# Optimization experiments

Measured on AMD Instinct MI355X. Metric: run time of the kernel, lower is better.

The kernel has to match this reference:

```python
import jax, jax.numpy as jnp
import numpy as np


def _base_index(H, W, dtype=jnp.float32):
    # Homogeneous pixel coordinates (x, y, 1) per pixel, shape [H, W, 3].
    x = jnp.arange(W, dtype=dtype)
    y = jnp.arange(H, dtype=dtype)
    xx, yy = jnp.meshgrid(x, y)  # [H, W]
    return jnp.stack([xx, yy, jnp.ones_like(xx)], axis=-1)


def _bilinear_resample(image, coords):
    # image: [B, H, W, C]; coords: [B, H, W, 2] in (x, y) order (tf resampler convention).
    # Out-of-bounds corners contribute zero (zero padding), matching tfa.image.resampler.
    B, H, W, C = image.shape
    x = coords[..., 0]
    y = coords[..., 1]
    x0 = jnp.floor(x)
    y0 = jnp.floor(y)
    wx1 = x - x0
    wy1 = y - y0
    wx0 = 1.0 - wx1
    wy0 = 1.0 - wy1
    x0i = x0.astype(jnp.int32)
    y0i = y0.astype(jnp.int32)
    x1i = x0i + 1
    y1i = y0i + 1

    def corner(yi, xi, w):
        valid = (xi >= 0) & (xi < W) & (yi >= 0) & (yi < H)
        xc = jnp.clip(xi, 0, W - 1)
        yc = jnp.clip(yi, 0, H - 1)
        # gather per batch: [B, H, W, C]
        g = jax.vmap(lambda im, yy, xx: im[yy, xx])(image, yc, xc)
        return g * (w * valid.astype(image.dtype))[..., None]

    return (corner(y0i, x0i, wy0 * wx0) + corner(y0i, x1i, wy0 * wx1)
            + corner(y1i, x0i, wy1 * wx0) + corner(y1i, x1i, wy1 * wx1))


def setup_inputs() -> dict:
    key = jax.random.key(0)
    k1, k2, k3 = jax.random.split(key, 3)
    B, H, W, C = 4, 512, 640, 16
    image_tensor = jax.random.normal(k1, (B, H, W, C), dtype=jnp.float32)
    # positive depths around 1
    depth_tensor = 0.5 + jax.random.uniform(k2, (B, H, W), dtype=jnp.float32)
    # near-identity projective transform so sampled coords land mostly in-bounds
    eye = jnp.eye(4, dtype=jnp.float32)[None].repeat(B, axis=0)
    project_tensor = eye + 0.001 * jax.random.normal(k3, (B, 4, 4), dtype=jnp.float32)
    return {"image_tensor": image_tensor, "depth_tensor": depth_tensor,
            "project_tensor": project_tensor}


def reference(image_tensor, depth_tensor, project_tensor):
    B, H, W, C = image_tensor.shape
    base = _base_index(H, W, image_tensor.dtype)  # [H, W, 3]
    R = project_tensor[:, :3, :3]                 # [B, 3, 3]
    t = project_tensor[:, :3, 3]                  # [B, 3]
    # tf.tensordot(R, base, [-1,-1]) -> [B,3,H,W]; transpose -> [B,H,W,3]
    rotate = jnp.einsum('bij,hwj->bhwi', R, base)
    sample = rotate * depth_tensor[..., None] + t[:, None, None, :]  # [B,H,W,3]
    coords = sample[..., :2] / sample[..., 2:3]                       # [B,H,W,2] (x,y)
    return _bilinear_resample(image_tensor, coords)
```

## Files before the change

kernel.cpp:

```cpp
#include <hip/hip_runtime.h>

constexpr int B  = 4;
constexpr int H  = 512;
constexpr int Wd = 640;
constexpr int C  = 16;
constexpr int NPIX = B * H * Wd;
constexpr int NTHREADS = NPIX * (C / 4);

__global__ __launch_bounds__(256) void depth_project_kernel(
    const float* __restrict__ image,
    const float* __restrict__ depth,
    const float* __restrict__ proj,
    float4* __restrict__ out)
{
    int tid = blockIdx.x * blockDim.x + threadIdx.x;
    if (tid >= NTHREADS) return;

    int c4  = tid & 3;
    int pix = tid >> 2;
    int w   = pix % Wd;
    int t   = pix / Wd;
    int h   = t % H;
    int b   = t / H;

    const float* P = proj + b * 16;
    float x = (float)w;
    float y = (float)h;
    float d = depth[pix];

    float sx = (P[0] * x + P[1] * y + P[2])  * d + P[3];
    float sy = (P[4] * x + P[5] * y + P[6])  * d + P[7];
    float sz = (P[8] * x + P[9] * y + P[10]) * d + P[11];
    float cx = sx / sz;
    float cy = sy / sz;

    float x0f = floorf(cx), y0f = floorf(cy);
    float wx1 = cx - x0f,   wy1 = cy - y0f;
    float wx0 = 1.0f - wx1, wy0 = 1.0f - wy1;
    int x0 = (int)x0f, y0 = (int)y0f;
    int x1 = x0 + 1,   y1 = y0 + 1;

    float vx0 = (x0 >= 0 && x0 < Wd) ? 1.0f : 0.0f;
    float vx1 = (x1 >= 0 && x1 < Wd) ? 1.0f : 0.0f;
    float vy0 = (y0 >= 0 && y0 < H)  ? 1.0f : 0.0f;
    float vy1 = (y1 >= 0 && y1 < H)  ? 1.0f : 0.0f;

    int x0c = min(max(x0, 0), Wd - 1);
    int x1c = min(max(x1, 0), Wd - 1);
    int y0c = min(max(y0, 0), H - 1);
    int y1c = min(max(y1, 0), H - 1);

    float w00 = wy0 * wx0 * vy0 * vx0;
    float w01 = wy0 * wx1 * vy0 * vx1;
    float w10 = wy1 * wx0 * vy1 * vx0;
    float w11 = wy1 * wx1 * vy1 * vx1;

    const float4* img4 = (const float4*)image;
    int base_b = b * (H * Wd * 4);
    float4 g00 = img4[base_b + (y0c * Wd + x0c) * 4 + c4];
    float4 g01 = img4[base_b + (y0c * Wd + x1c) * 4 + c4];
    float4 g10 = img4[base_b + (y1c * Wd + x0c) * 4 + c4];
    float4 g11 = img4[base_b + (y1c * Wd + x1c) * 4 + c4];

    float4 r;
    r.x = g00.x * w00 + g01.x * w01 + g10.x * w10 + g11.x * w11;
    r.y = g00.y * w00 + g01.y * w01 + g10.y * w10 + g11.y * w11;
    r.z = g00.z * w00 + g01.z * w01 + g10.z * w10 + g11.z * w11;
    r.w = g00.w * w00 + g01.w * w01 + g10.w * w10 + g11.w * w11;

    out[tid] = r;
}

extern "C" void kernel_launch(void* const* d_in, const int* in_sizes, int n_in,
                              void* d_out, int out_size, void* d_ws, size_t ws_size,
                              hipStream_t stream) {
    const float* image = (const float*)d_in[0];
    const float* depth = (const float*)d_in[1];
    const float* proj  = (const float*)d_in[2];
    float4* out = (float4*)d_out;

    constexpr int block = 256;
    constexpr int grid  = (NTHREADS + block - 1) / block;
    depth_project_kernel<<<grid, block, 0, stream>>>(image, depth, proj, out);
}
```

Baseline: 157.7 us.

## Process all batches per thread with nontemporal depth loads and output stores

Each thread now handles one pixel/channel-quad for all four batch images, so the grid shrinks fourfold and the pixel index math is done once per thread. Coordinate computation for every batch is done first, then all sixteen gathers are issued together to raise memory-level parallelism. Depth loads and output stores use nontemporal hints so streaming data does not pollute the cache needed for image gathers. Risks are higher register use, lower occupancy, and nontemporal stores that may not suit the hardware.

Result: no change. 158.1 us (+0.2%).

```diff
diff --git a/kernel.cpp b/kernel.cpp
--- a/kernel.cpp
+++ b/kernel.cpp
@@ -3,9 +3,14 @@
 constexpr int B  = 4;
 constexpr int H  = 512;
 constexpr int Wd = 640;
-constexpr int C  = 16;
-constexpr int NPIX = B * H * Wd;
-constexpr int NTHREADS = NPIX * (C / 4);
+constexpr int NPIX_IMG = H * Wd;
+constexpr int BLOCK = 256;
+constexpr int PIX_PER_BLOCK  = BLOCK / 4;
+constexpr int BLOCKS_PER_ROW = Wd / PIX_PER_BLOCK;
+constexpr int GRID = H * BLOCKS_PER_ROW;
+static_assert(Wd % PIX_PER_BLOCK == 0, "block must tile a row exactly");
+
+typedef float f32x4 __attribute__((ext_vector_type(4)));
 
 __global__ __launch_bounds__(256) void depth_project_kernel(
     const float* __restrict__ image,
@@ -13,62 +18,86 @@
     const float* __restrict__ proj,
     float4* __restrict__ out)
 {
-    int tid = blockIdx.x * blockDim.x + threadIdx.x;
-    if (tid >= NTHREADS) return;
+    const int blk = blockIdx.x;
+    const int h  = blk / BLOCKS_PER_ROW;
+    const int wb = (blk % BLOCKS_PER_ROW) * PIX_PER_BLOCK;
 
-    int c4  = tid & 3;
-    int pix = tid >> 2;
-    int w   = pix % Wd;
-    int t   = pix / Wd;
-    int h   = t % H;
-    int b   = t / H;
+    const int tix = threadIdx.x;
+    const int c4  = tix & 3;
+    const int pl  = tix >> 2;
+    const int w   = wb + pl;
+    const int pix0 = h * Wd + w;
 
-    const float* P = proj + b * 16;
-    float x = (float)w;
-    float y = (float)h;
-    float d = depth[pix];
+    const float x = (float)w;
+    const float y = (float)h;
 
-    float sx = (P[0] * x + P[1] * y + P[2])  * d + P[3];
-    float sy = (P[4] * x + P[5] * y + P[6])  * d + P[7];
-    float sz = (P[8] * x + P[9] * y + P[10]) * d + P[11];
-    float cx = sx / sz;
-    float cy = sy / sz;
+    float d[B];
+#pragma unroll
+    for (int b = 0; b < B; ++b)
+        d[b] = __builtin_nontemporal_load(depth + b * NPIX_IMG + pix0);
 
-    float x0f = floorf(cx), y0f = floorf(cy);
-    float wx1 = cx - x0f,   wy1 = cy - y0f;
-    float wx0 = 1.0f - wx1, wy0 = 1.0f - wy1;
-    int x0 = (int)x0f, y0 = (int)y0f;
-    int x1 = x0 + 1,   y1 = y0 + 1;
+    float w00[B], w01[B], w10[B], w11[B];
+    int   k00[B], k01[B], k10[B], k11[B];
+#pragma unroll
+    for (int b = 0; b < B; ++b) {
+        const float* P = proj + b * 16;
 
-    float vx0 = (x0 >= 0 && x0 < Wd) ? 1.0f : 0.0f;
-    float vx1 = (x1 >= 0 && x1 < Wd) ? 1.0f : 0.0f;
-    float vy0 = (y0 >= 0 && y0 < H)  ? 1.0f : 0.0f;
-    float vy1 = (y1 >= 0 && y1 < H)  ? 1.0f : 0.0f;
+        float sx = (P[0] * x + P[1] * y + P[2])  * d[b] + P[3];
+        float sy = (P[4] * x + P[5] * y + P[6])  * d[b] + P[7];
+        float sz = (P[8] * x + P[9] * y + P[10]) * d[b] + P[11];
+        float cx = sx / sz;
+        float cy = sy / sz;
 
-    int x0c = min(max(x0, 0), Wd - 1);
-    int x1c = min(max(x1, 0), Wd - 1);
-    int y0c = min(max(y0, 0), H - 1);
-    int y1c = min(max(y1, 0), H - 1);
+        float x0f = floorf(cx), y0f = floorf(cy);
+        float wx1 = cx - x0f,   wy1 = cy - y0f;
+        float wx0 = 1.0f - wx1, wy0 = 1.0f - wy1;
+        int x0 = (int)x0f, y0 = (int)y0f;
+        int x1 = x0 + 1,   y1 = y0 + 1;
 
-    float w00 = wy0 * wx0 * vy0 * vx0;
-    float w01 = wy0 * wx1 * vy0 * vx1;
-    float w10 = wy1 * wx0 * vy1 * vx0;
-    float w11 = wy1 * wx1 * vy1 * vx1;
+        float vx0 = (x0 >= 0 && x0 < Wd) ? 1.0f : 0.0f;
+        float vx1 = (x1 >= 0 && x1 < Wd) ? 1.0f : 0.0f;
+        float vy0 = (y0 >= 0 && y0 < H)  ? 1.0f : 0.0f;
+        float vy1 = (y1 >= 0 && y1 < H)  ? 1.0f : 0.0f;
+
+        int x0c = min(max(x0, 0), Wd - 1);
+        int x1c = min(max(x1, 0), Wd - 1);
+        int y0c = min(max(y0, 0), H - 1);
+        int y1c = min(max(y1, 0), H - 1);
+
+        w00[b] = wy0 * wx0 * vy0 * vx0;
+        w01[b] = wy0 * wx1 * vy0 * vx1;
+        w10[b] = wy1 * wx0 * vy1 * vx0;
+        w11[b] = wy1 * wx1 * vy1 * vx1;
+
+        const int base_b = b * (NPIX_IMG * 4);
+        k00[b] = base_b + (y0c * Wd + x0c) * 4 + c4;
+        k01[b] = base_b + (y0c * Wd + x1c) * 4 + c4;
+        k10[b] = base_b + (y1c * Wd + x0c) * 4 + c4;
+        k11[b] = base_b + (y1c * Wd + x1c) * 4 + c4;
+    }
 
     const float4* img4 = (const float4*)image;
-    int base_b = b * (H * Wd * 4);
-    float4 g00 = img4[base_b + (y0c * Wd + x0c) * 4 + c4];
-    float4 g01 = img4[base_b + (y0c * Wd + x1c) * 4 + c4];
-    float4 g10 = img4[base_b + (y1c * Wd + x0c) * 4 + c4];
-    float4 g11 = img4[base_b + (y1c * Wd + x1c) * 4 + c4];
+    float4 r[B];
+#pragma unroll
+    for (int b = 0; b < B; ++b) {
+        float4 g00 = img4[k00[b]];
+        float4 g01 = img4[k01[b]];
+        float4 g10 = img4[k10[b]];
+        float4 g11 = img4[k11[b]];
+        float4 rr;
+        rr.x = g00.x * w00[b] + g01.x * w01[b] + g10.x * w10[b] + g11.x * w11[b];
+        rr.y = g00.y * w00[b] + g01.y * w01[b] + g10.y * w10[b] + g11.y * w11[b];
+        rr.z = g00.z * w00[b] + g01.z * w01[b] + g10.z * w10[b] + g11.z * w11[b];
+        rr.w = g00.w * w00[b] + g01.w * w01[b] + g10.w * w10[b] + g11.w * w11[b];
+        r[b] = rr;
+    }
 
-    float4 r;
-    r.x = g00.x * w00 + g01.x * w01 + g10.x * w10 + g11.x * w11;
-    r.y = g00.y * w00 + g01.y * w01 + g10.y * w10 + g11.y * w11;
-    r.z = g00.z * w00 + g01.z * w01 + g10.z * w10 + g11.z * w11;
-    r.w = g00.w * w00 + g01.w * w01 + g10.w * w10 + g11.w * w11;
-
-    out[tid] = r;
+    f32x4* out_v = (f32x4*)out;
+#pragma unroll
+    for (int b = 0; b < B; ++b) {
+        f32x4 v = { r[b].x, r[b].y, r[b].z, r[b].w };
+        __builtin_nontemporal_store(v, out_v + (b * NPIX_IMG + pix0) * 4 + c4);
+    }
 }
 
 extern "C" void kernel_launch(void* const* d_in, const int* in_sizes, int n_in,
@@ -79,7 +108,5 @@
     const float* proj  = (const float*)d_in[2];
     float4* out = (float4*)d_out;
 
-    constexpr int block = 256;
-    constexpr int grid  = (NTHREADS + block - 1) / block;
-    depth_project_kernel<<<grid, block, 0, stream>>>(image, depth, proj, out);
+    depth_project_kernel<<<GRID, BLOCK, 0, stream>>>(image, depth, proj, out);
 }
```
